# Performance work log

Measured on AMD Instinct MI355X. Metric: run time of the kernel, lower is better.

## Reference

```python
import jax, jax.numpy as jnp
import numpy as np

DIM = 128
RES = 64
H_SP, W_SP = 64, 4   # idx == 0: H_sp = resolution, W_sp = split_size
NUM_HEADS = 4
HEAD_DIM = DIM // NUM_HEADS
SCALE = HEAD_DIM ** -0.5


def img2windows(img, H_sp, W_sp):
    # img: (B, C, H, W) -> (B*nHw*nWw, H_sp*W_sp, C)
    B, C, H, W = img.shape
    x = img.reshape(B, C, H // H_sp, H_sp, W // W_sp, W_sp)
    x = jnp.transpose(x, (0, 2, 4, 3, 5, 1))
    return x.reshape(-1, H_sp * W_sp, C)


def windows2img(wins, H_sp, W_sp, H, W):
    C = wins.shape[-1]
    B = wins.shape[0] // ((H // H_sp) * (W // W_sp))
    x = wins.reshape(B, H // H_sp, W // W_sp, H_sp, W_sp, C)
    x = jnp.transpose(x, (0, 5, 1, 3, 2, 4))
    return x.reshape(B, C, H, W)


def im2cswin(x, H_sp, W_sp, num_heads):
    # (B, C, H, W) -> (B', num_heads, L, head_dim)
    C = x.shape[1]
    w = img2windows(x, H_sp, W_sp)                       # (B', L, C)
    w = w.reshape(-1, H_sp * W_sp, num_heads, C // num_heads)
    return jnp.transpose(w, (0, 2, 1, 3))


def conv1x1(x, w, b):
    # x: (B, C, H, W), w: (O, C), b: (O,)
    return jnp.einsum('bchw,oc->bohw', x, w) + b[None, :, None, None]


def depthwise5x5(x, w, b):
    # x: (B, C, H, W), w: (C, 1, 5, 5) depthwise, pad=2
    y = jax.lax.conv_general_dilated(
        x, w, window_strides=(1, 1), padding=((2, 2), (2, 2)),
        feature_group_count=x.shape[1],
        dimension_numbers=('NCHW', 'OIHW', 'NCHW'))
    return y + b[None, :, None, None]


def setup_inputs() -> dict:
    key = jax.random.key(0)
    ks = jax.random.split(key, 8)
    B = 16
    x = jax.random.normal(ks[0], (B, DIM, RES, RES), dtype=jnp.float32)
    n_windows = B * (RES // H_SP) * (RES // W_SP)
    L = H_SP * W_SP
    attn_input = jax.random.normal(ks[1], (n_windows, NUM_HEADS, L, L), dtype=jnp.float32)
    s = 0.02
    wq = jax.random.normal(ks[2], (DIM, DIM), dtype=jnp.float32) * s
    bq = jnp.zeros((DIM,), dtype=jnp.float32)
    wv = jax.random.normal(ks[3], (DIM, DIM), dtype=jnp.float32) * s
    bv = jnp.zeros((DIM,), dtype=jnp.float32)
    w_lepe = jax.random.normal(ks[4], (DIM, 1, 5, 5), dtype=jnp.float32) * s
    b_lepe = jnp.zeros((DIM,), dtype=jnp.float32)
    temperature = jnp.ones((NUM_HEADS, 1, 1), dtype=jnp.float32)
    return {"x": x, "attn_input": attn_input, "wq": wq, "bq": bq,
            "wv": wv, "bv": bv, "w_lepe": w_lepe, "b_lepe": b_lepe,
            "temperature": temperature}


def reference(x, attn_input, wq, bq, wv, bv, w_lepe, b_lepe, temperature):
    B, C, H, W = x.shape
    v_map = conv1x1(x, wv, bv)
    lepe = depthwise5x5(v_map, w_lepe, b_lepe)           # (B, C, H, W)
    # shift_size == 0: no roll
    q_map = conv1x1(x, wq, bq)
    q = im2cswin(q_map + lepe, H_SP, W_SP, NUM_HEADS) * SCALE  # (B', nh, L, d)
    k = im2cswin(x + lepe, H_SP, W_SP, NUM_HEADS)
    v = im2cswin(v_map, H_SP, W_SP, NUM_HEADS)
    scores = jnp.einsum('whqd,whkd->whqk', q, k)         # (B', nh, L, L)
    attn = jax.nn.softmax(scores, axis=-1) + temperature[None] * attn_input
    out = jnp.einsum('whqk,whkd->whqd', attn, v)         # (B', nh, L, d)
    out = jnp.transpose(out, (0, 2, 1, 3)).reshape(-1, H_SP * W_SP, C)
    out = windows2img(out, H_SP, W_SP, H, W)             # (B, C, H, W)
    return (out + lepe, attn)
```

## Files before the change

### kernel.cpp

```cpp
#include <hip/hip_runtime.h>

typedef __attribute__((ext_vector_type(4)))  float fx4;
typedef __attribute__((ext_vector_type(16))) float fx16;
typedef __attribute__((ext_vector_type(8)))  short bf8;
typedef __attribute__((ext_vector_type(4)))  unsigned int u32x4;

#define SCALE 0.17677669529663687f

__device__ __forceinline__ unsigned short f2bf(float f) {
  unsigned int u = __builtin_bit_cast(unsigned int, f);
  unsigned int r = (u + 0x7fffu + ((u >> 16) & 1u)) >> 16;
  return (unsigned short)r;
}
__device__ __forceinline__ float bf2f(unsigned short u) {
  unsigned int v = ((unsigned int)u) << 16;
  return __builtin_bit_cast(float, v);
}

__global__ __launch_bounds__(256) void k01_qv(const float* __restrict__ x,
    const float* __restrict__ wq, const float* __restrict__ bq,
    const float* __restrict__ wv, const float* __restrict__ bv,
    unsigned short* __restrict__ xT, unsigned short* __restrict__ qT,
    unsigned short* __restrict__ vT) {
  int pt = blockIdx.x, b = blockIdx.y, t = threadIdx.x;
  __shared__ unsigned short tT[128 * 136];
  const float* xb = x + (size_t)b * 524288 + pt * 128;
#pragma unroll
  for (int i = 0; i < 16; ++i) {
    int slot = t + i * 256;
    int c = slot >> 5, p4 = slot & 31;
    float4 v = *reinterpret_cast<const float4*>(xb + (size_t)c * 4096 + p4 * 4);
    unsigned short* q = &tT[(p4 * 4) * 136 + c];
    q[0] = f2bf(v.x); q[136] = f2bf(v.y); q[272] = f2bf(v.z); q[408] = f2bf(v.w);
  }
  __syncthreads();
  {
    int pix = t >> 1, hf = t & 1;
    unsigned short tmp[64];
#pragma unroll
    for (int j = 0; j < 64; ++j) tmp[j] = tT[pix * 136 + hf * 64 + j];
    unsigned short* dst = xT + ((size_t)b * 4096 + pt * 128 + pix) * 128 + hf * 64;
#pragma unroll
    for (int q = 0; q < 8; ++q)
      *reinterpret_cast<bf8*>(dst + q * 8) = *reinterpret_cast<bf8*>(tmp + q * 8);
  }
  int lane = t & 63, wave = t >> 6;
  int wm = wave >> 1, wn = wave & 1;
  int l31 = lane & 31, g2 = lane >> 5;
#pragma unroll
  for (int qv = 0; qv < 2; ++qv) {
    const float* W = qv ? wv : wq;
    const float* bias = qv ? bv : bq;
    unsigned short* out = qv ? vT : qT;
    fx16 acc[2][2] = {};
#pragma unroll
    for (int ks = 0; ks < 8; ++ks) {
      int kbase = ks * 16 + g2 * 8;
      bf8 a[2], bb[2];
#pragma unroll
      for (int mi = 0; mi < 2; ++mi) {
        int pix = (wm * 2 + mi) * 32 + l31;
        a[mi] = *reinterpret_cast<const bf8*>(&tT[pix * 136 + kbase]);
      }
#pragma unroll
      for (int ni = 0; ni < 2; ++ni) {
        int oc = (wn * 2 + ni) * 32 + l31;
        const float* wp = W + oc * 128 + kbase;
        float4 w0 = *reinterpret_cast<const float4*>(wp);
        float4 w1 = *reinterpret_cast<const float4*>(wp + 4);
        bf8 r;
        r[0]=(short)f2bf(w0.x); r[1]=(short)f2bf(w0.y); r[2]=(short)f2bf(w0.z); r[3]=(short)f2bf(w0.w);
        r[4]=(short)f2bf(w1.x); r[5]=(short)f2bf(w1.y); r[6]=(short)f2bf(w1.z); r[7]=(short)f2bf(w1.w);
        bb[ni] = r;
      }
#pragma unroll
      for (int mi = 0; mi < 2; ++mi)
#pragma unroll
        for (int ni = 0; ni < 2; ++ni)
          acc[mi][ni] = __builtin_amdgcn_mfma_f32_32x32x16_bf16(a[mi], bb[ni], acc[mi][ni], 0, 0, 0);
    }
#pragma unroll
    for (int ni = 0; ni < 2; ++ni) {
      int oc = (wn * 2 + ni) * 32 + l31;
      float bsv = bias[oc];
#pragma unroll
      for (int mi = 0; mi < 2; ++mi) {
#pragma unroll
        for (int r = 0; r < 16; ++r) {
          int row = (r & 3) + 8 * (r >> 2) + 4 * g2;
          int pix = pt * 128 + (wm * 2 + mi) * 32 + row;
          out[((size_t)b * 4096 + pix) * 128 + oc] = f2bf(acc[mi][ni][r] + bsv);
        }
      }
    }
  }
}

__global__ __launch_bounds__(256) void k2_lepe(const unsigned short* __restrict__ vT,
    const float* __restrict__ wl5, const float* __restrict__ bl,
    unsigned short* __restrict__ lepe,
    unsigned short* __restrict__ kT_io, unsigned short* __restrict__ qT_io) {
  int strip = blockIdx.x, hd = blockIdx.y, b = blockIdx.z;
  int t = threadIdx.x;
  __shared__ unsigned short tile[12 * 64 * 34];
  int h0 = strip * 8;
#pragma unroll
  for (int i = 0; i < 12; ++i) {
    int slot = t + i * 256;
    int r = slot >> 8;
    int rem = slot & 255;
    int w = rem >> 2, cc = rem & 3;
    int h = h0 - 2 + r;
    unsigned short vv[8];
    if (h >= 0 && h < 64) {
      *reinterpret_cast<bf8*>(vv) = *reinterpret_cast<const bf8*>(
          vT + ((size_t)b * 4096 + h * 64 + w) * 128 + hd * 32 + cc * 8);
    } else {
#pragma unroll
      for (int j = 0; j < 8; ++j) vv[j] = 0;
    }
    unsigned int* dst = reinterpret_cast<unsigned int*>(&tile[(r * 64 + w) * 34 + cc * 8]);
#pragma unroll
    for (int j = 0; j < 4; ++j)
      dst[j] = ((unsigned int)vv[2 * j + 1] << 16) | (unsigned int)vv[2 * j];
  }
  __syncthreads();
  int c2 = t & 15, w16 = t >> 4;
  int c = c2 * 2;
  float wt0[25], wt1[25];
#pragma unroll
  for (int i = 0; i < 25; ++i) {
    wt0[i] = wl5[(hd * 32 + c) * 25 + i];
    wt1[i] = wl5[(hd * 32 + c + 1) * 25 + i];
  }
  float b0 = bl[hd * 32 + c], b1 = bl[hd * 32 + c + 1];
  for (int hh = 0; hh < 8; ++hh) {
    for (int wi = 0; wi < 4; ++wi) {
      int w = w16 * 4 + wi;
      float a0 = b0, a1 = b1;
#pragma unroll
      for (int dy = 0; dy < 5; ++dy) {
        int rr = hh + dy;
#pragma unroll
        for (int dx = 0; dx < 5; ++dx) {
          int wx = w + dx - 2;
          if (wx < 0 || wx >= 64) continue;
          unsigned int pr = *reinterpret_cast<const unsigned int*>(&tile[(rr * 64 + wx) * 34 + c]);
          float v0 = bf2f((unsigned short)(pr & 0xffffu));
          float v1 = bf2f((unsigned short)(pr >> 16));
          a0 += v0 * wt0[dy * 5 + dx];
          a1 += v1 * wt1[dy * 5 + dx];
        }
      }
      size_t po = ((size_t)b * 4096 + (h0 + hh) * 64 + w) * 128 + hd * 32 + c;
      unsigned int lp = (unsigned int)f2bf(a0) | ((unsigned int)f2bf(a1) << 16);
      *reinterpret_cast<unsigned int*>(&lepe[po]) = lp;
      unsigned int kx = *reinterpret_cast<const unsigned int*>(&kT_io[po]);
      unsigned int qx = *reinterpret_cast<const unsigned int*>(&qT_io[po]);
      unsigned int kn = (unsigned int)f2bf(bf2f((unsigned short)(kx & 0xffffu)) + a0)
                      | ((unsigned int)f2bf(bf2f((unsigned short)(kx >> 16)) + a1) << 16);
      unsigned int qn = (unsigned int)f2bf((bf2f((unsigned short)(qx & 0xffffu)) + a0) * SCALE)
                      | ((unsigned int)f2bf((bf2f((unsigned short)(qx >> 16)) + a1) * SCALE) << 16);
      *reinterpret_cast<unsigned int*>(&kT_io[po]) = kn;
      *reinterpret_cast<unsigned int*>(&qT_io[po]) = qn;
    }
  }
}

__global__ __launch_bounds__(256, 4) void k3_attn(
    const unsigned short* __restrict__ kT, const unsigned short* __restrict__ qS,
    const unsigned short* __restrict__ vT,
    const float* __restrict__ ai, const float* __restrict__ temp,
    float* __restrict__ attn, unsigned short* __restrict__ out_win) {
  int w = blockIdx.x;
  int hd = blockIdx.y;
  int b = w >> 4, ww = w & 15;
  int t = threadIdx.x, lane = t & 63, wave = t >> 6;
  int l15 = lane & 15, g = (lane >> 4) & 3;
  __shared__ unsigned short Kf[16 * 4 * 16 * 8];
  __shared__ unsigned short Vf[16 * 4 * 16 * 8];
  __shared__ float Stg[4 * 512];

  const size_t aBase = ((size_t)w * 4 + hd) * 65536;
  const float* aiB = ai + aBase;
  float* atB = attn + aBase;
  unsigned short* owB = out_win + ((size_t)w * 4 + hd) * 8192;

  fx4 av[8];
  {
    int qrow0 = wave * 16 + l15;
    const fx4* aiRow0 = reinterpret_cast<const fx4*>(aiB + (size_t)qrow0 * 256 + g * 4);
#pragma unroll
    for (int nt = 0; nt < 8; ++nt) av[nt] = aiRow0[nt * 4];
  }
  asm volatile("" ::: "memory");

  {
    int row = t;
    int pix = (row >> 2) * 64 + ww * 4 + (row & 3);
    const unsigned short* src = kT + ((size_t)b * 4096 + pix) * 128 + hd * 32;
    int nt = row >> 4, sl = row & 15;
#pragma unroll
    for (int gg = 0; gg < 4; ++gg)
      *reinterpret_cast<bf8*>(&Kf[((nt * 4 + gg) * 16 + sl) * 8]) =
          *reinterpret_cast<const bf8*>(src + gg * 8);
  }
  {
    int row = t;
    int pix = (row >> 2) * 64 + ww * 4 + (row & 3);
    const unsigned short* src = vT + ((size_t)b * 4096 + pix) * 128 + hd * 32;
    unsigned short vv[32];
#pragma unroll
    for (int q = 0; q < 4; ++q)
      *reinterpret_cast<bf8*>(vv + q * 8) = *reinterpret_cast<const bf8*>(src + q * 8);
    int ks = row >> 5, gg = (row >> 3) & 3, j = row & 7;
#pragma unroll
    for (int d = 0; d < 32; ++d)
      Vf[(((ks * 2 + (d >> 4)) * 4 + gg) * 16 + (d & 15)) * 8 + j] = vv[d];
  }
  __syncthreads();
  float tHd = temp[hd];

  int srcA = l15 + ((lane & 16) << 1);
  int srcB = srcA + 16;
  bool ghi = (lane >= 32);
  float* Sw = Stg + wave * 512;

  for (int pass = 0; pass < 4; ++pass) {
    int qbase = (pass * 4 + wave) * 16;
    int qrow = qbase + l15;
    const fx4* aiRow = reinterpret_cast<const fx4*>(aiB + (size_t)qrow * 256 + g * 4);

    bf8 qf;
    {
      int pix = (qrow >> 2) * 64 + ww * 4 + (qrow & 3);
      qf = *reinterpret_cast<const bf8*>(
          qS + ((size_t)b * 4096 + pix) * 128 + hd * 32 + g * 8);
    }

    fx4 acc[16];
#pragma unroll
    for (int nt = 0; nt < 16; ++nt) {
      bf8 kfr = *reinterpret_cast<const bf8*>(&Kf[((nt * 4 + g) * 16 + l15) * 8]);
      fx4 z; z[0] = 0.f; z[1] = 0.f; z[2] = 0.f; z[3] = 0.f;
      acc[nt] = __builtin_amdgcn_mfma_f32_16x16x32_bf16(kfr, qf, z, 0, 0, 0);
    }

    float m0 = fmaxf(acc[0][0], acc[0][1]), m1 = fmaxf(acc[0][2], acc[0][3]);
    float m2 = fmaxf(acc[1][0], acc[1][1]), m3 = fmaxf(acc[1][2], acc[1][3]);
#pragma unroll
    for (int nt = 2; nt < 16; nt += 2) {
      m0 = fmaxf(m0, fmaxf(acc[nt][0], acc[nt][1]));
      m1 = fmaxf(m1, fmaxf(acc[nt][2], acc[nt][3]));
      m2 = fmaxf(m2, fmaxf(acc[nt + 1][0], acc[nt + 1][1]));
      m3 = fmaxf(m3, fmaxf(acc[nt + 1][2], acc[nt + 1][3]));
    }
    float m = fmaxf(fmaxf(m0, m1), fmaxf(m2, m3));
    m = fmaxf(m, __shfl_xor(m, 16));
    m = fmaxf(m, __shfl_xor(m, 32));

    float s0 = 0.f, s1 = 0.f, s2 = 0.f, s3 = 0.f;
#pragma unroll
    for (int nt = 0; nt < 16; ++nt) {
      float p0 = __expf(acc[nt][0] - m);
      float p1 = __expf(acc[nt][1] - m);
      float p2 = __expf(acc[nt][2] - m);
      float p3 = __expf(acc[nt][3] - m);
      acc[nt][0] = p0; acc[nt][1] = p1; acc[nt][2] = p2; acc[nt][3] = p3;
      s0 += p0; s1 += p1; s2 += p2; s3 += p3;
    }
    float s = (s0 + s1) + (s2 + s3);
    s += __shfl_xor(s, 16);
    s += __shfl_xor(s, 32);
    float inv = 1.0f / s;

    fx4 av2[8];
#pragma unroll
    for (int nt = 0; nt < 8; ++nt) av2[nt] = aiRow[(8 + nt) * 4];
    asm volatile("" ::: "memory");

    unsigned int pp0[16], pp1[16];
#pragma unroll
    for (int p = 0; p < 8; ++p) {
#pragma unroll
      for (int u = 0; u < 2; ++u) {
        int nt = 2 * p + u;
        fx4 a4 = (nt < 8) ? av[nt] : av2[nt - 8];
        fx4 sv;
        sv[0] = acc[nt][0] * inv + tHd * a4[0];
        sv[1] = acc[nt][1] * inv + tHd * a4[1];
        sv[2] = acc[nt][2] * inv + tHd * a4[2];
        sv[3] = acc[nt][3] * inv + tHd * a4[3];
        int pc = (g + 4 * u) ^ (l15 & 7);
        *reinterpret_cast<fx4*>(&Sw[l15 * 32 + pc * 4]) = sv;
        pp0[nt] = (unsigned int)f2bf(sv[0]) | ((unsigned int)f2bf(sv[1]) << 16);
        pp1[nt] = (unsigned int)f2bf(sv[2]) | ((unsigned int)f2bf(sv[3]) << 16);
      }
#pragma unroll
      for (int i = 0; i < 2; ++i) {
        int r = (lane >> 3) + 8 * i;
        int cf = lane & 7;
        int pc = cf ^ (r & 7);
        fx4 v = *reinterpret_cast<const fx4*>(&Sw[r * 32 + pc * 4]);
        __builtin_nontemporal_store(v,
            reinterpret_cast<fx4*>(atB + (size_t)(qbase + r) * 256 + p * 32 + cf * 4));
      }
    }

    if (pass < 3) {
      int qrowN = ((pass + 1) * 4 + wave) * 16 + l15;
      const fx4* aiRowN = reinterpret_cast<const fx4*>(aiB + (size_t)qrowN * 256 + g * 4);
#pragma unroll
      for (int nt = 0; nt < 8; ++nt) av[nt] = aiRowN[nt * 4];
      asm volatile("" ::: "memory");
    }

    fx4 oT[2];
    oT[0][0]=0.f;oT[0][1]=0.f;oT[0][2]=0.f;oT[0][3]=0.f;
    oT[1][0]=0.f;oT[1][1]=0.f;oT[1][2]=0.f;oT[1][3]=0.f;
#pragma unroll
    for (int c = 0; c < 8; ++c) {
      int n0 = 2 * c, n1 = 2 * c + 1;
      unsigned int x0 = (unsigned int)__shfl((int)pp0[n0], srcA);
      unsigned int y0 = (unsigned int)__shfl((int)pp0[n1], srcA);
      unsigned int x1 = (unsigned int)__shfl((int)pp1[n0], srcA);
      unsigned int y1 = (unsigned int)__shfl((int)pp1[n1], srcA);
      unsigned int x2 = (unsigned int)__shfl((int)pp0[n0], srcB);
      unsigned int y2 = (unsigned int)__shfl((int)pp0[n1], srcB);
      unsigned int x3 = (unsigned int)__shfl((int)pp1[n0], srcB);
      unsigned int y3 = (unsigned int)__shfl((int)pp1[n1], srcB);
      u32x4 bw;
      bw[0] = ghi ? y0 : x0;
      bw[1] = ghi ? y1 : x1;
      bw[2] = ghi ? y2 : x2;
      bw[3] = ghi ? y3 : x3;
      bf8 pf = __builtin_bit_cast(bf8, bw);
#pragma unroll
      for (int dblk = 0; dblk < 2; ++dblk) {
        bf8 vf = *reinterpret_cast<const bf8*>(&Vf[(((c * 2 + dblk) * 4 + g) * 16 + l15) * 8]);
        oT[dblk] = __builtin_amdgcn_mfma_f32_16x16x32_bf16(vf, pf, oT[dblk], 0, 0, 0);
      }
    }
#pragma unroll
    for (int dblk = 0; dblk < 2; ++dblk) {
      unsigned int w0 = (unsigned int)f2bf(oT[dblk][0]) | ((unsigned int)f2bf(oT[dblk][1]) << 16);
      unsigned int w1 = (unsigned int)f2bf(oT[dblk][2]) | ((unsigned int)f2bf(oT[dblk][3]) << 16);
      uint2 st; st.x = w0; st.y = w1;
      *reinterpret_cast<uint2*>(&owB[(size_t)qrow * 32 + dblk * 16 + g * 4]) = st;
    }
  }
}

__global__ __launch_bounds__(256) void k4_out(const unsigned short* __restrict__ out_win,
    const unsigned short* __restrict__ lepe, float* __restrict__ out0) {
  int h = blockIdx.x, b = blockIdx.y, t = threadIdx.x;
  __shared__ float winb[16 * 533];
  __shared__ float lep[64 * 129];
#pragma unroll
  for (int i = 0; i < 4; ++i) {
    int slot = t + i * 256;
    int ww = slot >> 6, rem = slot & 63;
    int hdq = rem >> 4, rem2 = rem & 15;
    int wl = rem2 >> 2, dq = rem2 & 3;
    bf8 v = *reinterpret_cast<const bf8*>(
        out_win + (((size_t)(b * 16 + ww) * 4 + hdq) * 256 + h * 4 + wl) * 32 + dq * 8);
    float* p = &winb[ww * 533 + wl * 133 + hdq * 33 + dq * 8];
#pragma unroll
    for (int j = 0; j < 8; ++j) p[j] = bf2f((unsigned short)v[j]);
  }
#pragma unroll
  for (int i = 0; i < 4; ++i) {
    int slot = t + i * 256;
    int w = slot >> 4, cq = slot & 15;
    bf8 lv = *reinterpret_cast<const bf8*>(
        lepe + ((size_t)b * 4096 + h * 64 + w) * 128 + cq * 8);
    float* p = &lep[w * 129 + cq * 8];
#pragma unroll
    for (int j = 0; j < 8; ++j) p[j] = bf2f((unsigned short)lv[j]);
  }
  __syncthreads();
  int w = t & 63, cg = t >> 6;
#pragma unroll
  for (int ci = 0; ci < 32; ++ci) {
    int c = cg * 32 + ci;
    float val = winb[(w >> 2) * 533 + (w & 3) * 133 + (c >> 5) * 33 + (c & 31)] + lep[w * 129 + c];
    out0[((size_t)(b * 128 + c) * 64 + h) * 64 + w] = val;
  }
}

extern "C" void kernel_launch(void* const* d_in, const int* in_sizes, int n_in,
                              void* d_out, int out_size, void* d_ws, size_t ws_size,
                              hipStream_t stream) {
  const float* x    = (const float*)d_in[0];
  const float* ai   = (const float*)d_in[1];
  const float* wq   = (const float*)d_in[2];
  const float* bq   = (const float*)d_in[3];
  const float* wv   = (const float*)d_in[4];
  const float* bv   = (const float*)d_in[5];
  const float* wl5  = (const float*)d_in[6];
  const float* bl   = (const float*)d_in[7];
  const float* temp = (const float*)d_in[8];
  float* out0 = (float*)d_out;
  float* attn = out0 + 8388608;

  char* ws = (char*)d_ws;
  unsigned short* xT = (unsigned short*)(ws);
  unsigned short* qT = (unsigned short*)(ws + 16777216);
  unsigned short* vT = (unsigned short*)(ws + 33554432);
  unsigned short* lepe = (unsigned short*)(ws + 50331648);
  unsigned short* ow = (unsigned short*)(ws + 83886080);

  k01_qv <<<dim3(32, 16),   256, 0, stream>>>(x, wq, bq, wv, bv, xT, qT, vT);
  k2_lepe<<<dim3(8, 4, 16), 256, 0, stream>>>(vT, wl5, bl, lepe, xT, qT);
  k3_attn<<<dim3(256, 4),   256, 0, stream>>>(xT, qT, vT, ai, temp, attn, ow);
  k4_out <<<dim3(64, 16),   256, 0, stream>>>(ow, lepe, out0);
}
```

Measured before the change: 250.3 us.

## Fuse lepe addition into attention loads and shrink lepe strip height

The lepe kernel no longer reads and rewrites the K and Q buffers. It only writes lepe, and the attention kernel now adds lepe while loading K into shared memory and Q into registers, applying the scale to Q there. The lepe strip height is halved and the grid doubled, which gives more blocks but more redundant halo loads. This removes a read-modify-write pass over two 16 MB bf16 buffers in exchange for extra lepe loads and conversion math inside the attention kernel.

```diff
diff --git a/kernel.cpp b/kernel.cpp
--- a/kernel.cpp
+++ b/kernel.cpp
@@ -98,14 +98,13 @@
 
 __global__ __launch_bounds__(256) void k2_lepe(const unsigned short* __restrict__ vT,
     const float* __restrict__ wl5, const float* __restrict__ bl,
-    unsigned short* __restrict__ lepe,
-    unsigned short* __restrict__ kT_io, unsigned short* __restrict__ qT_io) {
+    unsigned short* __restrict__ lepe) {
   int strip = blockIdx.x, hd = blockIdx.y, b = blockIdx.z;
   int t = threadIdx.x;
-  __shared__ unsigned short tile[12 * 64 * 34];
-  int h0 = strip * 8;
-#pragma unroll
-  for (int i = 0; i < 12; ++i) {
+  __shared__ unsigned short tile[8 * 64 * 34];
+  int h0 = strip * 4;
+#pragma unroll
+  for (int i = 0; i < 8; ++i) {
     int slot = t + i * 256;
     int r = slot >> 8;
     int rem = slot & 255;
@@ -134,7 +133,7 @@
     wt1[i] = wl5[(hd * 32 + c + 1) * 25 + i];
   }
   float b0 = bl[hd * 32 + c], b1 = bl[hd * 32 + c + 1];
-  for (int hh = 0; hh < 8; ++hh) {
+  for (int hh = 0; hh < 4; ++hh) {
     for (int wi = 0; wi < 4; ++wi) {
       int w = w16 * 4 + wi;
       float a0 = b0, a1 = b1;
@@ -155,21 +154,13 @@
       size_t po = ((size_t)b * 4096 + (h0 + hh) * 64 + w) * 128 + hd * 32 + c;
       unsigned int lp = (unsigned int)f2bf(a0) | ((unsigned int)f2bf(a1) << 16);
       *reinterpret_cast<unsigned int*>(&lepe[po]) = lp;
-      unsigned int kx = *reinterpret_cast<const unsigned int*>(&kT_io[po]);
-      unsigned int qx = *reinterpret_cast<const unsigned int*>(&qT_io[po]);
-      unsigned int kn = (unsigned int)f2bf(bf2f((unsigned short)(kx & 0xffffu)) + a0)
-                      | ((unsigned int)f2bf(bf2f((unsigned short)(kx >> 16)) + a1) << 16);
-      unsigned int qn = (unsigned int)f2bf((bf2f((unsigned short)(qx & 0xffffu)) + a0) * SCALE)
-                      | ((unsigned int)f2bf((bf2f((unsigned short)(qx >> 16)) + a1) * SCALE) << 16);
-      *reinterpret_cast<unsigned int*>(&kT_io[po]) = kn;
-      *reinterpret_cast<unsigned int*>(&qT_io[po]) = qn;
     }
   }
 }
 
 __global__ __launch_bounds__(256, 4) void k3_attn(
     const unsigned short* __restrict__ kT, const unsigned short* __restrict__ qS,
-    const unsigned short* __restrict__ vT,
+    const unsigned short* __restrict__ vT, const unsigned short* __restrict__ lepe,
     const float* __restrict__ ai, const float* __restrict__ temp,
     float* __restrict__ attn, unsigned short* __restrict__ out_win) {
   int w = blockIdx.x;
@@ -198,12 +189,20 @@
   {
     int row = t;
     int pix = (row >> 2) * 64 + ww * 4 + (row & 3);
-    const unsigned short* src = kT + ((size_t)b * 4096 + pix) * 128 + hd * 32;
+    size_t off = ((size_t)b * 4096 + pix) * 128 + hd * 32;
+    const unsigned short* src = kT + off;
+    const unsigned short* lsrc = lepe + off;
     int nt = row >> 4, sl = row & 15;
 #pragma unroll
-    for (int gg = 0; gg < 4; ++gg)
-      *reinterpret_cast<bf8*>(&Kf[((nt * 4 + gg) * 16 + sl) * 8]) =
-          *reinterpret_cast<const bf8*>(src + gg * 8);
+    for (int gg = 0; gg < 4; ++gg) {
+      bf8 kx = *reinterpret_cast<const bf8*>(src + gg * 8);
+      bf8 lx = *reinterpret_cast<const bf8*>(lsrc + gg * 8);
+      bf8 r;
+#pragma unroll
+      for (int j = 0; j < 8; ++j)
+        r[j] = (short)f2bf(bf2f((unsigned short)kx[j]) + bf2f((unsigned short)lx[j]));
+      *reinterpret_cast<bf8*>(&Kf[((nt * 4 + gg) * 16 + sl) * 8]) = r;
+    }
   }
   {
     int row = t;
@@ -234,8 +233,12 @@
     bf8 qf;
     {
       int pix = (qrow >> 2) * 64 + ww * 4 + (qrow & 3);
-      qf = *reinterpret_cast<const bf8*>(
-          qS + ((size_t)b * 4096 + pix) * 128 + hd * 32 + g * 8);
+      size_t off = ((size_t)b * 4096 + pix) * 128 + hd * 32 + g * 8;
+      bf8 qx = *reinterpret_cast<const bf8*>(qS + off);
+      bf8 lx = *reinterpret_cast<const bf8*>(lepe + off);
+#pragma unroll
+      for (int j = 0; j < 8; ++j)
+        qf[j] = (short)f2bf((bf2f((unsigned short)qx[j]) + bf2f((unsigned short)lx[j])) * SCALE);
     }
 
     fx4 acc[16];
@@ -410,8 +413,8 @@
   unsigned short* lepe = (unsigned short*)(ws + 50331648);
   unsigned short* ow = (unsigned short*)(ws + 83886080);
 
-  k01_qv <<<dim3(32, 16),   256, 0, stream>>>(x, wq, bq, wv, bv, xT, qT, vT);
-  k2_lepe<<<dim3(8, 4, 16), 256, 0, stream>>>(vT, wl5, bl, lepe, xT, qT);
-  k3_attn<<<dim3(256, 4),   256, 0, stream>>>(xT, qT, vT, ai, temp, attn, ow);
-  k4_out <<<dim3(64, 16),   256, 0, stream>>>(ow, lepe, out0);
-}
+  k01_qv <<<dim3(32, 16),    256, 0, stream>>>(x, wq, bq, wv, bv, xT, qT, vT);
+  k2_lepe<<<dim3(16, 4, 16), 256, 0, stream>>>(vT, wl5, bl, lepe);
+  k3_attn<<<dim3(256, 4),    256, 0, stream>>>(xT, qT, vT, lepe, ai, temp, attn, ow);
+  k4_out <<<dim3(64, 16),    256, 0, stream>>>(ow, lepe, out0);
+}
```

After: 235.2 us. -6.0%, faster.
